# Kernel tuning notes

Measured on AMD Instinct MI355X. Metric: run time of the kernel, lower is better.

The kernel has to match this reference:

```python
import jax, jax.numpy as jnp
import numpy as np

B, L, H, E, D = 4, 2048, 8, 64, 64  # seq S == L (causal mask requires square scores)


def setup_inputs() -> dict:
    key = jax.random.key(0)
    k0, k1, k2, k3, k4 = jax.random.split(key, 5)
    queries = jax.random.normal(k0, (B, L, H, E), jnp.float32)
    keys = jax.random.normal(k1, (B, L, H, E), jnp.float32)
    values = jax.random.normal(k2, (B, L, H, D), jnp.float32)
    # per-sample learned de-stationary scale (positive) and bias
    tau = jax.random.uniform(k3, (B, 1, 1), jnp.float32, 0.5, 1.5)
    delta = jax.random.normal(k4, (B, 1, L), jnp.float32) * 0.1
    return {"queries": queries, "keys": keys, "values": values, "tau": tau, "delta": delta}


def reference(queries, keys, values, tau, delta):
    Bq, Lq, Hq, Eq = queries.shape
    S = keys.shape[1]
    scale = 1.0 / jnp.sqrt(jnp.asarray(Eq, jnp.float32))
    # torch path: rearrange('b s h d l -> (b d) s h l') with s=h=d=1 -> [B,1,1,1] / [B,1,1,S]
    tau_b = tau.reshape(Bq, 1, 1, 1)
    delta_b = delta.reshape(Bq, 1, 1, -1)[..., :S]
    # scores: [B, H, L, S]
    scores = jnp.einsum('blhe,bshe->bhls', queries, keys) * tau_b + delta_b
    causal = jnp.triu(jnp.ones((Lq, S), bool), k=1)  # True above diagonal -> masked
    scores = jnp.where(causal, -jnp.inf, scores)
    A = jax.nn.softmax(scale * scores, axis=-1)  # dropout is identity in eval/reference
    V = jnp.einsum('bhls,bshd->blhd', A, values)  # [B, L, H, D]
    return V
```

## Files before the change

kernel.cpp:

```cpp
#include <hip/hip_runtime.h>
#include <hip/hip_bf16.h>

#define Bsz 4
#define Lsz 2048
#define Hsz 8

typedef __attribute__((ext_vector_type(8)))  short bf16x8;
typedef __attribute__((ext_vector_type(4)))  short bf16x4;
typedef __attribute__((ext_vector_type(4)))  float f32x4;

__device__ __forceinline__ short f2bs(float f) {
    union { float f; unsigned u; } v; v.f = f;
    unsigned r = v.u + 0x7FFFu + ((v.u >> 16) & 1u);
    return (short)(r >> 16);
}
__device__ __forceinline__ short f2bs_rh(float f) {
    return (short)((__float_as_uint(f) + 0x8000u) >> 16);
}

__device__ __forceinline__ void stage16(const short* g, short* l) {
    __builtin_amdgcn_global_load_lds(
        (const __attribute__((address_space(1))) unsigned int*)g,
        (__attribute__((address_space(3))) unsigned int*)l,
        16, 0, 0);
}

__global__ __launch_bounds__(256) void prep_kv(
    const float* __restrict__ ksrc, const float* __restrict__ vsrc,
    short* __restrict__ Kf, short* __restrict__ Vf)
{
    __shared__ float Tl[64][65];
    const int raw = blockIdx.x;
    const int tid = threadIdx.x;
    const bool isK = raw < Bsz*Hsz*32;
    const int bid = isK ? raw : raw - Bsz*Hsz*32;
    const int tl = bid & 31, bh = bid >> 5;
    const int b = bh >> 3, h = bh & 7;

    const int row = tid >> 2, c0 = (tid & 3) * 16;
    const float* src = (isK ? ksrc : vsrc)
                     + (((size_t)b*Lsz + tl*64 + row)*Hsz + h)*64 + c0;
    *(float4*)&Tl[row][c0]      = *(const float4*)(src);
    *(float4*)&Tl[row][c0 + 4]  = *(const float4*)(src + 4);
    *(float4*)&Tl[row][c0 + 8]  = *(const float4*)(src + 8);
    *(float4*)&Tl[row][c0 + 12] = *(const float4*)(src + 12);
    __syncthreads();

    const int lane = tid & 63, ln = lane & 15, quad = lane >> 4;
    if (isK) {
        short* dst = Kf + (size_t)bid * 4096;
        #pragma unroll
        for (int cc = 0; cc < 2; ++cc) {
            const int c  = (tid >> 6)*2 + cc;
            const int kq = c >> 1, eb = c & 1;
            const float* rp = &Tl[kq*16 + ln][eb*32 + quad*8];
            bf16x8 o = {f2bs(rp[0]),f2bs(rp[1]),f2bs(rp[2]),f2bs(rp[3]),
                        f2bs(rp[4]),f2bs(rp[5]),f2bs(rp[6]),f2bs(rp[7])};
            *(bf16x8*)(dst + c*512 + lane*8) = o;
        }
    } else {
        short* dst = Vf + (size_t)bid * 4096;
        #pragma unroll
        for (int cc = 0; cc < 2; ++cc) {
            const int c   = (tid >> 6)*2 + cc;
            const int kq  = c >> 1, dgp = c & 1;
            const int s0  = kq*16 + quad*4;
            const int d0  = dgp*32 + ln;
            const int d1  = dgp*32 + 16 + ln;
            bf16x8 o = {f2bs(Tl[s0+0][d0]), f2bs(Tl[s0+1][d0]),
                        f2bs(Tl[s0+2][d0]), f2bs(Tl[s0+3][d0]),
                        f2bs(Tl[s0+0][d1]), f2bs(Tl[s0+1][d1]),
                        f2bs(Tl[s0+2][d1]), f2bs(Tl[s0+3][d1])};
            *(bf16x8*)(dst + c*512 + lane*8) = o;
        }
    }
}

__global__ __launch_bounds__(256, 3) void dsattn_main(
    const float* __restrict__ q,
    const short* __restrict__ Kf,
    const short* __restrict__ Vf,
    const float* __restrict__ tau,
    const float* __restrict__ delta,
    float* __restrict__ out)
{
    __shared__ __align__(16) short Kb[2][4096];
    __shared__ __align__(16) short Vb[2][4096];
    __shared__ float dls[Lsz];

    const int tid  = threadIdx.x;
    const int kq   = tid >> 6;
    const int lane = tid & 63;
    const int ln   = lane & 15;
    const int quad = lane >> 4;

    const int bh = blockIdx.x;
    const int b  = bh >> 3, h = bh & 7;
    const int y = blockIdx.y, g8 = y >> 3, a = y & 7;
    const int qt = (g8 == 0) ? 31 - 2*a : (g8 == 1) ? 2*a
                 : (g8 == 2) ? 30 - 2*a : 2*a + 1;
    const int q0 = qt * 64;
    const int T  = qt + 1;

    const float c2  = 0.125f * 1.44269504f;
    const float st2 = c2 * tau[b];

    const short* gK = Kf + (size_t)bh*(32*4096) + kq*1024 + lane*8;
    const short* gV = Vf + (size_t)bh*(32*4096) + kq*1024 + lane*8;

    short* const myK0 = &Kb[0][kq*1024];
    short* const myV0 = &Vb[0][kq*1024];

#define STAGE(buf) do {                                                     \
        short* k_ = (buf) ? myK0 + 4096 : myK0;                             \
        short* v_ = (buf) ? myV0 + 4096 : myV0;                             \
        stage16(gK + 0*512, k_ + 0*512);                                    \
        stage16(gK + 1*512, k_ + 1*512);                                    \
        stage16(gV + 0*512, v_ + 0*512);                                    \
        stage16(gV + 1*512, v_ + 1*512);                                    \
        gK += 4096; gV += 4096;                                             \
        __builtin_amdgcn_sched_barrier(0);                                  \
    } while (0)
#define WAITN(n) do {                                                       \
        asm volatile("s_waitcnt vmcnt(" #n ")" ::: "memory");               \
        __builtin_amdgcn_sched_barrier(0);                                  \
    } while (0)

    STAGE(0);

    {
        const float* dsrc = delta + (size_t)b*Lsz + tid*8;
        float4 av = *(const float4*)(dsrc);
        float4 cv = *(const float4*)(dsrc + 4);
        av.x*=c2; av.y*=c2; av.z*=c2; av.w*=c2;
        cv.x*=c2; cv.y*=c2; cv.z*=c2; cv.w*=c2;
        *(float4*)&dls[tid*8]     = av;
        *(float4*)&dls[tid*8 + 4] = cv;
    }

    bf16x8 qf[4][2];
    #pragma unroll
    for (int qg = 0; qg < 4; ++qg) {
        const float* qrow = q + (((size_t)b*Lsz + q0 + qg*16 + ln)*Hsz + h)*64;
        float4 a0 = *(const float4*)(qrow + quad*8);
        float4 a1 = *(const float4*)(qrow + quad*8 + 4);
        float4 b0 = *(const float4*)(qrow + 32 + quad*8);
        float4 b1 = *(const float4*)(qrow + 32 + quad*8 + 4);
        qf[qg][0] = (bf16x8){f2bs(a0.x),f2bs(a0.y),f2bs(a0.z),f2bs(a0.w),
                             f2bs(a1.x),f2bs(a1.y),f2bs(a1.z),f2bs(a1.w)};
        qf[qg][1] = (bf16x8){f2bs(b0.x),f2bs(b0.y),f2bs(b0.z),f2bs(b0.w),
                             f2bs(b1.x),f2bs(b1.y),f2bs(b1.z),f2bs(b1.w)};
    }

    f32x4 oacc[4][4];
    #pragma unroll
    for (int dg = 0; dg < 4; ++dg)
        #pragma unroll
        for (int qg = 0; qg < 4; ++qg)
            oacc[dg][qg] = (f32x4){0.f,0.f,0.f,0.f};
    float l_acc[4] = {0.f,0.f,0.f,0.f};

    __syncthreads();

#define TILE_BODY(t_, MASKED, HASNEXT) do {                                 \
        const short* Kc_ = ((t_) & 1) ? myK0 + 4096 : myK0;                 \
        const short* Vc_ = ((t_) & 1) ? myV0 + 4096 : myV0;                 \
        if (HASNEXT) STAGE(((t_)+1) & 1);                                   \
        if (HASNEXT) WAITN(6); else WAITN(2);            \
        bf16x8 kf0_ = *(const bf16x8*)(Kc_ + 0*512 + lane*8);               \
        bf16x8 kf1_ = *(const bf16x8*)(Kc_ + 1*512 + lane*8);               \
        f32x4 sacc_[4];                                                     \
        __builtin_amdgcn_s_setprio(1);                                      \
        _Pragma("unroll")                                                   \
        for (int qg = 0; qg < 4; ++qg) {                                    \
            f32x4 z_ = (f32x4){0.f,0.f,0.f,0.f};                            \
            z_ = __builtin_amdgcn_mfma_f32_16x16x32_bf16(kf0_, qf[qg][0], z_, 0,0,0); \
            sacc_[qg] = __builtin_amdgcn_mfma_f32_16x16x32_bf16(kf1_, qf[qg][1], z_, 0,0,0); \
        }                                                                   \
        __builtin_amdgcn_s_setprio(0);                                      \
        if (MASKED) {                                                       \
            _Pragma("unroll")                                               \
            for (int qg = 0; qg < 4; ++qg)                                  \
                _Pragma("unroll")                                           \
                for (int r = 0; r < 4; ++r)                                 \
                    if (kq*16 + quad*4 + r > qg*16 + ln) sacc_[qg][r] = -1e30f; \
        }                                                                   \
        f32x4 dlv_ = *(const f32x4*)&dls[(t_)*64 + kq*16 + quad*4];         \
        bf16x4 pT_[4];                                                      \
        _Pragma("unroll")                                                   \
        for (int qg = 0; qg < 4; ++qg) {                                    \
            float p0_ = __builtin_amdgcn_exp2f(fmaf(sacc_[qg][0], st2, dlv_[0])); \
            float p1_ = __builtin_amdgcn_exp2f(fmaf(sacc_[qg][1], st2, dlv_[1])); \
            float p2_ = __builtin_amdgcn_exp2f(fmaf(sacc_[qg][2], st2, dlv_[2])); \
            float p3_ = __builtin_amdgcn_exp2f(fmaf(sacc_[qg][3], st2, dlv_[3])); \
            l_acc[qg] += (p0_ + p1_) + (p2_ + p3_);                         \
            pT_[qg] = (bf16x4){f2bs_rh(p0_), f2bs_rh(p1_),                  \
                               f2bs_rh(p2_), f2bs_rh(p3_)};                 \
        }                                                                   \
        if (HASNEXT) WAITN(4); else WAITN(0);            \
        bf16x8 vv0_ = *(const bf16x8*)(Vc_ + 0*512 + lane*8);               \
        bf16x8 vv1_ = *(const bf16x8*)(Vc_ + 1*512 + lane*8);               \
        bf16x4 vf_[4];                                                      \
        vf_[0] = (bf16x4){vv0_[0], vv0_[1], vv0_[2], vv0_[3]};              \
        vf_[1] = (bf16x4){vv0_[4], vv0_[5], vv0_[6], vv0_[7]};              \
        vf_[2] = (bf16x4){vv1_[0], vv1_[1], vv1_[2], vv1_[3]};              \
        vf_[3] = (bf16x4){vv1_[4], vv1_[5], vv1_[6], vv1_[7]};              \
        __builtin_amdgcn_s_setprio(1);                                      \
        _Pragma("unroll")                                                   \
        for (int dg = 0; dg < 4; ++dg)                                      \
            _Pragma("unroll")                                               \
            for (int qg = 0; qg < 4; ++qg)                                  \
                oacc[dg][qg] = __builtin_amdgcn_mfma_f32_16x16x16bf16_1k(   \
                    vf_[dg], pT_[qg], oacc[dg][qg], 0,0,0);                 \
        __builtin_amdgcn_s_setprio(0);                                      \
    } while (0)

    for (int t = 0; t < T - 1; ++t) TILE_BODY(t, false, true);
    TILE_BODY(T - 1, true, false);

    float lq[4];
    #pragma unroll
    for (int qg = 0; qg < 4; ++qg) {
        float s = l_acc[qg];
        s += __shfl_xor(s, 16, 64);
        s += __shfl_xor(s, 32, 64);
        lq[qg] = s;
    }
    float* KbF = (float*)&Kb[0][0];
    float* VbF = (float*)&Vb[0][0];
    float* lred = dls;
    __syncthreads();

    if (lane < 16)
        #pragma unroll
        for (int qg = 0; qg < 4; ++qg) lred[kq*64 + qg*16 + ln] = lq[qg];
    if (kq == 1 || kq == 3) {
        float* dst = (kq == 1) ? KbF : VbF;
        #pragma unroll
        for (int dg = 0; dg < 4; ++dg)
            #pragma unroll
            for (int qg = 0; qg < 4; ++qg)
                *(f32x4*)(dst + (dg*4+qg)*256 + lane*4) = oacc[dg][qg];
    }
    __syncthreads();
    if (kq == 0 || kq == 2) {
        const float* srcp = (kq == 0) ? KbF : VbF;
        #pragma unroll
        for (int dg = 0; dg < 4; ++dg)
            #pragma unroll
            for (int qg = 0; qg < 4; ++qg) {
                f32x4 v = *(const f32x4*)(srcp + (dg*4+qg)*256 + lane*4);
                oacc[dg][qg][0] += v[0]; oacc[dg][qg][1] += v[1];
                oacc[dg][qg][2] += v[2]; oacc[dg][qg][3] += v[3];
            }
    }
    __syncthreads();
    if (kq == 2) {
        #pragma unroll
        for (int dg = 0; dg < 4; ++dg)
            #pragma unroll
            for (int qg = 0; qg < 4; ++qg)
                *(f32x4*)(KbF + (dg*4+qg)*256 + lane*4) = oacc[dg][qg];
    }
    __syncthreads();
    if (kq == 0) {
        float inv[4];
        #pragma unroll
        for (int qg = 0; qg < 4; ++qg)
            inv[qg] = 1.0f / (lred[qg*16 + ln] + lred[64 + qg*16 + ln]
                            + lred[128 + qg*16 + ln] + lred[192 + qg*16 + ln]);
        #pragma unroll
        for (int qg = 0; qg < 4; ++qg) {
            float* orow = out + (((size_t)b*Lsz + q0 + qg*16 + ln)*Hsz + h)*64;
            #pragma unroll
            for (int dg = 0; dg < 4; ++dg) {
                f32x4 v = *(const f32x4*)(KbF + (dg*4+qg)*256 + lane*4);
                float4 o = {(oacc[dg][qg][0] + v[0]) * inv[qg],
                            (oacc[dg][qg][1] + v[1]) * inv[qg],
                            (oacc[dg][qg][2] + v[2]) * inv[qg],
                            (oacc[dg][qg][3] + v[3]) * inv[qg]};
                *(float4*)(orow + dg*16 + quad*4) = o;
            }
        }
    }
#undef STAGE
#undef WAITN
#undef TILE_BODY
}

extern "C" void kernel_launch(void* const* d_in, const int* in_sizes, int n_in,
                              void* d_out, int out_size, void* d_ws, size_t ws_size,
                              hipStream_t stream) {
    (void)in_sizes; (void)n_in; (void)out_size; (void)ws_size;
    const float* q     = (const float*)d_in[0];
    const float* k     = (const float*)d_in[1];
    const float* v     = (const float*)d_in[2];
    const float* tau   = (const float*)d_in[3];
    const float* delta = (const float*)d_in[4];
    float* out = (float*)d_out;

    short* Kf = (short*)d_ws;
    short* Vf = (short*)d_ws + (size_t)(4*1024*1024);

    prep_kv<<<dim3(Bsz*Hsz*32*2), dim3(256), 0, stream>>>(k, v, Kf, Vf);
    dsattn_main<<<dim3(Bsz*Hsz, 32), dim3(256), 0, stream>>>(q, Kf, Vf, tau, delta, out);
}
```

Measured before the change: 130.4 us.

## Fuse K/V bf16 conversion into attention kernel, dropping prep pass

Removes the separate prep kernel that converted K/V to bf16 MFMA layout in a workspace. The attention kernel now loads fp32 K and V directly from global memory per tile, converts them in registers, and keeps Q in LDS instead of registers. This saves a launch and the workspace write/read. In exchange it loses the async LDS double-buffered prefetch, reads twice the bytes with strided scalar V loads, and repeats the conversion in every query tile.

```diff
diff --git a/kernel.cpp b/kernel.cpp
--- a/kernel.cpp
+++ b/kernel.cpp
@@ -18,75 +18,17 @@
     return (short)((__float_as_uint(f) + 0x8000u) >> 16);
 }
 
-__device__ __forceinline__ void stage16(const short* g, short* l) {
-    __builtin_amdgcn_global_load_lds(
-        (const __attribute__((address_space(1))) unsigned int*)g,
-        (__attribute__((address_space(3))) unsigned int*)l,
-        16, 0, 0);
-}
-
-__global__ __launch_bounds__(256) void prep_kv(
-    const float* __restrict__ ksrc, const float* __restrict__ vsrc,
-    short* __restrict__ Kf, short* __restrict__ Vf)
-{
-    __shared__ float Tl[64][65];
-    const int raw = blockIdx.x;
-    const int tid = threadIdx.x;
-    const bool isK = raw < Bsz*Hsz*32;
-    const int bid = isK ? raw : raw - Bsz*Hsz*32;
-    const int tl = bid & 31, bh = bid >> 5;
-    const int b = bh >> 3, h = bh & 7;
-
-    const int row = tid >> 2, c0 = (tid & 3) * 16;
-    const float* src = (isK ? ksrc : vsrc)
-                     + (((size_t)b*Lsz + tl*64 + row)*Hsz + h)*64 + c0;
-    *(float4*)&Tl[row][c0]      = *(const float4*)(src);
-    *(float4*)&Tl[row][c0 + 4]  = *(const float4*)(src + 4);
-    *(float4*)&Tl[row][c0 + 8]  = *(const float4*)(src + 8);
-    *(float4*)&Tl[row][c0 + 12] = *(const float4*)(src + 12);
-    __syncthreads();
-
-    const int lane = tid & 63, ln = lane & 15, quad = lane >> 4;
-    if (isK) {
-        short* dst = Kf + (size_t)bid * 4096;
-        #pragma unroll
-        for (int cc = 0; cc < 2; ++cc) {
-            const int c  = (tid >> 6)*2 + cc;
-            const int kq = c >> 1, eb = c & 1;
-            const float* rp = &Tl[kq*16 + ln][eb*32 + quad*8];
-            bf16x8 o = {f2bs(rp[0]),f2bs(rp[1]),f2bs(rp[2]),f2bs(rp[3]),
-                        f2bs(rp[4]),f2bs(rp[5]),f2bs(rp[6]),f2bs(rp[7])};
-            *(bf16x8*)(dst + c*512 + lane*8) = o;
-        }
-    } else {
-        short* dst = Vf + (size_t)bid * 4096;
-        #pragma unroll
-        for (int cc = 0; cc < 2; ++cc) {
-            const int c   = (tid >> 6)*2 + cc;
-            const int kq  = c >> 1, dgp = c & 1;
-            const int s0  = kq*16 + quad*4;
-            const int d0  = dgp*32 + ln;
-            const int d1  = dgp*32 + 16 + ln;
-            bf16x8 o = {f2bs(Tl[s0+0][d0]), f2bs(Tl[s0+1][d0]),
-                        f2bs(Tl[s0+2][d0]), f2bs(Tl[s0+3][d0]),
-                        f2bs(Tl[s0+0][d1]), f2bs(Tl[s0+1][d1]),
-                        f2bs(Tl[s0+2][d1]), f2bs(Tl[s0+3][d1])};
-            *(bf16x8*)(dst + c*512 + lane*8) = o;
-        }
-    }
-}
-
-__global__ __launch_bounds__(256, 3) void dsattn_main(
+__global__ __launch_bounds__(256, 3) void dsattn_fused(
     const float* __restrict__ q,
-    const short* __restrict__ Kf,
-    const short* __restrict__ Vf,
+    const float* __restrict__ ksrc,
+    const float* __restrict__ vsrc,
     const float* __restrict__ tau,
     const float* __restrict__ delta,
     float* __restrict__ out)
 {
-    __shared__ __align__(16) short Kb[2][4096];
-    __shared__ __align__(16) short Vb[2][4096];
     __shared__ float dls[Lsz];
+    __shared__ __align__(16) short Qs[4096];
+    __shared__ __align__(16) float Ored[2][4096];
 
     const int tid  = threadIdx.x;
     const int kq   = tid >> 6;
@@ -104,29 +46,6 @@
 
     const float c2  = 0.125f * 1.44269504f;
     const float st2 = c2 * tau[b];
-
-    const short* gK = Kf + (size_t)bh*(32*4096) + kq*1024 + lane*8;
-    const short* gV = Vf + (size_t)bh*(32*4096) + kq*1024 + lane*8;
-
-    short* const myK0 = &Kb[0][kq*1024];
-    short* const myV0 = &Vb[0][kq*1024];
-
-#define STAGE(buf) do {                                                     \
-        short* k_ = (buf) ? myK0 + 4096 : myK0;                             \
-        short* v_ = (buf) ? myV0 + 4096 : myV0;                             \
-        stage16(gK + 0*512, k_ + 0*512);                                    \
-        stage16(gK + 1*512, k_ + 1*512);                                    \
-        stage16(gV + 0*512, v_ + 0*512);                                    \
-        stage16(gV + 1*512, v_ + 1*512);                                    \
-        gK += 4096; gV += 4096;                                             \
-        __builtin_amdgcn_sched_barrier(0);                                  \
-    } while (0)
-#define WAITN(n) do {                                                       \
-        asm volatile("s_waitcnt vmcnt(" #n ")" ::: "memory");               \
-        __builtin_amdgcn_sched_barrier(0);                                  \
-    } while (0)
-
-    STAGE(0);
 
     {
         const float* dsrc = delta + (size_t)b*Lsz + tid*8;
@@ -138,19 +57,22 @@
         *(float4*)&dls[tid*8 + 4] = cv;
     }
 
-    bf16x8 qf[4][2];
-    #pragma unroll
-    for (int qg = 0; qg < 4; ++qg) {
-        const float* qrow = q + (((size_t)b*Lsz + q0 + qg*16 + ln)*Hsz + h)*64;
+    {
+        const float* qrow = q + (((size_t)b*Lsz + q0 + kq*16 + ln)*Hsz + h)*64;
         float4 a0 = *(const float4*)(qrow + quad*8);
         float4 a1 = *(const float4*)(qrow + quad*8 + 4);
         float4 b0 = *(const float4*)(qrow + 32 + quad*8);
         float4 b1 = *(const float4*)(qrow + 32 + quad*8 + 4);
-        qf[qg][0] = (bf16x8){f2bs(a0.x),f2bs(a0.y),f2bs(a0.z),f2bs(a0.w),
-                             f2bs(a1.x),f2bs(a1.y),f2bs(a1.z),f2bs(a1.w)};
-        qf[qg][1] = (bf16x8){f2bs(b0.x),f2bs(b0.y),f2bs(b0.z),f2bs(b0.w),
-                             f2bs(b1.x),f2bs(b1.y),f2bs(b1.z),f2bs(b1.w)};
-    }
+        bf16x8 q0f = {f2bs(a0.x),f2bs(a0.y),f2bs(a0.z),f2bs(a0.w),
+                      f2bs(a1.x),f2bs(a1.y),f2bs(a1.z),f2bs(a1.w)};
+        bf16x8 q1f = {f2bs(b0.x),f2bs(b0.y),f2bs(b0.z),f2bs(b0.w),
+                      f2bs(b1.x),f2bs(b1.y),f2bs(b1.z),f2bs(b1.w)};
+        *(bf16x8*)(&Qs[(kq*2+0)*512 + lane*8]) = q0f;
+        *(bf16x8*)(&Qs[(kq*2+1)*512 + lane*8]) = q1f;
+    }
+
+    const float* kp = ksrc + (((size_t)b*Lsz + kq*16 + ln)*Hsz + h)*64 + quad*8;
+    const float* vp = vsrc + (((size_t)b*Lsz + kq*16 + quad*4)*Hsz + h)*64 + ln;
 
     f32x4 oacc[4][4];
     #pragma unroll
@@ -162,20 +84,32 @@
 
     __syncthreads();
 
-#define TILE_BODY(t_, MASKED, HASNEXT) do {                                 \
-        const short* Kc_ = ((t_) & 1) ? myK0 + 4096 : myK0;                 \
-        const short* Vc_ = ((t_) & 1) ? myV0 + 4096 : myV0;                 \
-        if (HASNEXT) STAGE(((t_)+1) & 1);                                   \
-        if (HASNEXT) WAITN(6); else WAITN(2);            \
-        bf16x8 kf0_ = *(const bf16x8*)(Kc_ + 0*512 + lane*8);               \
-        bf16x8 kf1_ = *(const bf16x8*)(Kc_ + 1*512 + lane*8);               \
+#define TILE_BODY(t_, MASKED) do {                                          \
+        \
+        const float4 ka0_ = *(const float4*)(kp);                           \
+        const float4 ka1_ = *(const float4*)(kp + 4);                       \
+        const float4 kb0_ = *(const float4*)(kp + 32);                      \
+        const float4 kb1_ = *(const float4*)(kp + 36);                      \
+        float vs_[16];                                                      \
+        _Pragma("unroll")                                                   \
+        for (int dg = 0; dg < 4; ++dg)                                      \
+            _Pragma("unroll")                                               \
+            for (int j = 0; j < 4; ++j)                                     \
+                vs_[dg*4+j] = vp[j*512 + dg*16];                            \
+          \
+        bf16x8 kf0_ = {f2bs(ka0_.x),f2bs(ka0_.y),f2bs(ka0_.z),f2bs(ka0_.w),\
+                       f2bs(ka1_.x),f2bs(ka1_.y),f2bs(ka1_.z),f2bs(ka1_.w)};\
+        bf16x8 kf1_ = {f2bs(kb0_.x),f2bs(kb0_.y),f2bs(kb0_.z),f2bs(kb0_.w),\
+                       f2bs(kb1_.x),f2bs(kb1_.y),f2bs(kb1_.z),f2bs(kb1_.w)};\
         f32x4 sacc_[4];                                                     \
         __builtin_amdgcn_s_setprio(1);                                      \
         _Pragma("unroll")                                                   \
         for (int qg = 0; qg < 4; ++qg) {                                    \
+            bf16x8 qa_ = *(const bf16x8*)(&Qs[(qg*2+0)*512 + lane*8]);      \
+            bf16x8 qb_ = *(const bf16x8*)(&Qs[(qg*2+1)*512 + lane*8]);      \
             f32x4 z_ = (f32x4){0.f,0.f,0.f,0.f};                            \
-            z_ = __builtin_amdgcn_mfma_f32_16x16x32_bf16(kf0_, qf[qg][0], z_, 0,0,0); \
-            sacc_[qg] = __builtin_amdgcn_mfma_f32_16x16x32_bf16(kf1_, qf[qg][1], z_, 0,0,0); \
+            z_ = __builtin_amdgcn_mfma_f32_16x16x32_bf16(kf0_, qa_, z_, 0,0,0); \
+            sacc_[qg] = __builtin_amdgcn_mfma_f32_16x16x32_bf16(kf1_, qb_, z_, 0,0,0); \
         }                                                                   \
         __builtin_amdgcn_s_setprio(0);                                      \
         if (MASKED) {                                                       \
@@ -197,14 +131,12 @@
             pT_[qg] = (bf16x4){f2bs_rh(p0_), f2bs_rh(p1_),                  \
                                f2bs_rh(p2_), f2bs_rh(p3_)};                 \
         }                                                                   \
-        if (HASNEXT) WAITN(4); else WAITN(0);            \
-        bf16x8 vv0_ = *(const bf16x8*)(Vc_ + 0*512 + lane*8);               \
-        bf16x8 vv1_ = *(const bf16x8*)(Vc_ + 1*512 + lane*8);               \
+                                \
         bf16x4 vf_[4];                                                      \
-        vf_[0] = (bf16x4){vv0_[0], vv0_[1], vv0_[2], vv0_[3]};              \
-        vf_[1] = (bf16x4){vv0_[4], vv0_[5], vv0_[6], vv0_[7]};              \
-        vf_[2] = (bf16x4){vv1_[0], vv1_[1], vv1_[2], vv1_[3]};              \
-        vf_[3] = (bf16x4){vv1_[4], vv1_[5], vv1_[6], vv1_[7]};              \
+        _Pragma("unroll")                                                   \
+        for (int dg = 0; dg < 4; ++dg)                                      \
+            vf_[dg] = (bf16x4){f2bs(vs_[dg*4+0]), f2bs(vs_[dg*4+1]),        \
+                               f2bs(vs_[dg*4+2]), f2bs(vs_[dg*4+3])};       \
         __builtin_amdgcn_s_setprio(1);                                      \
         _Pragma("unroll")                                                   \
         for (int dg = 0; dg < 4; ++dg)                                      \
@@ -213,10 +145,11 @@
                 oacc[dg][qg] = __builtin_amdgcn_mfma_f32_16x16x16bf16_1k(   \
                     vf_[dg], pT_[qg], oacc[dg][qg], 0,0,0);                 \
         __builtin_amdgcn_s_setprio(0);                                      \
+        kp += 32768; vp += 32768;                                           \
     } while (0)
 
-    for (int t = 0; t < T - 1; ++t) TILE_BODY(t, false, true);
-    TILE_BODY(T - 1, true, false);
+    for (int t = 0; t < T - 1; ++t) TILE_BODY(t, false);
+    TILE_BODY(T - 1, true);
 
     float lq[4];
     #pragma unroll
@@ -226,8 +159,8 @@
         s += __shfl_xor(s, 32, 64);
         lq[qg] = s;
     }
-    float* KbF = (float*)&Kb[0][0];
-    float* VbF = (float*)&Vb[0][0];
+    float* KbF = &Ored[0][0];
+    float* VbF = &Ored[1][0];
     float* lred = dls;
     __syncthreads();
 
@@ -283,15 +216,13 @@
             }
         }
     }
-#undef STAGE
-#undef WAITN
 #undef TILE_BODY
 }
 
 extern "C" void kernel_launch(void* const* d_in, const int* in_sizes, int n_in,
                               void* d_out, int out_size, void* d_ws, size_t ws_size,
                               hipStream_t stream) {
-    (void)in_sizes; (void)n_in; (void)out_size; (void)ws_size;
+    (void)in_sizes; (void)n_in; (void)out_size; (void)d_ws; (void)ws_size;
     const float* q     = (const float*)d_in[0];
     const float* k     = (const float*)d_in[1];
     const float* v     = (const float*)d_in[2];
@@ -299,9 +230,5 @@
     const float* delta = (const float*)d_in[4];
     float* out = (float*)d_out;
 
-    short* Kf = (short*)d_ws;
-    short* Vf = (short*)d_ws + (size_t)(4*1024*1024);
-
-    prep_kv<<<dim3(Bsz*Hsz*32*2), dim3(256), 0, stream>>>(k, v, Kf, Vf);
-    dsattn_main<<<dim3(Bsz*Hsz, 32), dim3(256), 0, stream>>>(q, Kf, Vf, tau, delta, out);
-}
+    dsattn_fused<<<dim3(Bsz*Hsz, 32), dim3(256), 0, stream>>>(q, k, v, tau, delta, out);
+}
```

New measurement: 138.9 us. +6.5%, slower.
